# Kernel tuning notes

Hardware: AMD Instinct MI355X
Metric: run time of the kernel (lower is better)

The kernel has to match this reference:

```python
import jax, jax.numpy as jnp
import numpy as np

N_HEADS = 16
HEAD_DIM = 128
ROPE_DIM = 64
ROPE_BASE = 10000.0


def _rope(x, base):
    # x: (B, H, S, dim) -- standard rotate-half RoPE, positions = arange(S)
    B, H, S, dim = x.shape
    inv_freq = 1.0 / (base ** (jnp.arange(0, dim, 2, dtype=jnp.float32) / dim))
    pos = jnp.arange(S, dtype=jnp.float32)
    freqs = pos[:, None] * inv_freq[None, :]                  # (S, dim/2)
    emb = jnp.concatenate([freqs, freqs], axis=-1)            # (S, dim)
    cos = jnp.cos(emb).astype(x.dtype)[None, None]
    sin = jnp.sin(emb).astype(x.dtype)[None, None]
    x1, x2 = x[..., : dim // 2], x[..., dim // 2 :]
    rot = jnp.concatenate([-x2, x1], axis=-1)
    return x * cos + rot * sin


def setup_inputs() -> dict:
    key = jax.random.key(0)
    ks = jax.random.split(key, 7)
    B, S, D = 2, 2048, 2048
    s = 0.02
    return {
        "x": jax.random.normal(ks[0], (B, S, D), jnp.float32),
        "Wq": jax.random.normal(ks[1], (D, N_HEADS * HEAD_DIM), jnp.float32) * s,
        "Wq_rope": jax.random.normal(ks[2], (D, N_HEADS * ROPE_DIM), jnp.float32) * s,
        "Wkv_down": jax.random.normal(ks[3], (D, 512), jnp.float32) * s,
        "Wkv_up": jax.random.normal(ks[4], (512, 2 * N_HEADS * HEAD_DIM), jnp.float32) * s,
        "Wk_rope": jax.random.normal(ks[5], (D, ROPE_DIM), jnp.float32) * s,
        "Wo": jax.random.normal(ks[6], (D, D), jnp.float32) * s,
    }


def reference(x, Wq, Wq_rope, Wkv_down, Wkv_up, Wk_rope, Wo):
    B, S, D = x.shape
    H, hd, rd = N_HEADS, HEAD_DIM, ROPE_DIM

    # content and decoupled-RoPE queries
    q_c = (x @ Wq).reshape(B, S, H, hd).transpose(0, 2, 1, 3)        # (B,H,S,hd)
    q_r = (x @ Wq_rope).reshape(B, S, H, rd).transpose(0, 2, 1, 3)   # (B,H,S,rd)
    q_r = _rope(q_r, ROPE_BASE)

    # low-rank KV latent + shared rope key
    c_kv = x @ Wkv_down                                              # (B,S,r)
    k_r = _rope((x @ Wk_rope)[:, None, :, :], ROPE_BASE)             # (B,1,S,rd)

    kv = c_kv @ Wkv_up                                               # (B,S,2*H*hd)
    k_c, v = jnp.split(kv, 2, axis=-1)
    k_c = k_c.reshape(B, S, H, hd).transpose(0, 2, 1, 3)             # (B,H,S,hd)
    v = v.reshape(B, S, H, hd).transpose(0, 2, 1, 3)                 # (B,H,S,hd)

    q_full = jnp.concatenate([q_c, q_r], axis=-1)                    # (B,H,S,hd+rd)
    k_full = jnp.concatenate([k_c, jnp.broadcast_to(k_r, (B, H, S, rd))], axis=-1)

    scale = 1.0 / np.sqrt(hd + rd).astype(np.float32)
    scores = jnp.einsum("bhqd,bhkd->bhqk", q_full, k_full) * scale   # (B,H,S,S)
    mask = jnp.tril(jnp.ones((S, S), dtype=bool))
    scores = jnp.where(mask[None, None], scores, jnp.finfo(scores.dtype).min)
    attn = jax.nn.softmax(scores, axis=-1)

    out = jnp.einsum("bhqk,bhkd->bhqd", attn, v)                     # (B,H,S,hd)
    out = out.transpose(0, 2, 1, 3).reshape(B, S, D)
    return out @ Wo
```

## Files before the change

### kernel.cpp

```cpp
#include <hip/hip_runtime.h>
#include <hip/hip_bf16.h>
#include <cstdint>
#include <cstddef>

typedef unsigned short u16;
typedef __attribute__((ext_vector_type(8))) short short8;
typedef __attribute__((ext_vector_type(4))) float f32x4;
typedef __attribute__((ext_vector_type(16))) float f32x16;

__device__ __forceinline__ u16 f2bf(float f) {
    union { float f; uint32_t u; } v; v.f = f;
    uint32_t u = v.u;
    return (u16)((u + 0x7fffu + ((u >> 16) & 1u)) >> 16);
}
__device__ __forceinline__ float bf2f(u16 u) {
    union { uint32_t u; float f; } v; v.u = ((uint32_t)u) << 16;
    return v.f;
}
__device__ __forceinline__ float exp2_hw(float x) {
    float r;
    asm("v_exp_f32 %0, %1" : "=v"(r) : "v"(x));
    return r;
}
__device__ __forceinline__ uint32_t cvtpk(float lo, float hi) {
    uint32_t r;
    asm("v_cvt_pk_bf16_f32 %0, %1, %2" : "=v"(r) : "v"(lo), "v"(hi));
    return r;
}
__device__ __forceinline__ void permswap(uint32_t& a, uint32_t& b) {
    asm("v_permlane32_swap_b32 %0, %1" : "+v"(a), "+v"(b));
}
__device__ __forceinline__ float xhalf_max(float x) {
    union { float f; uint32_t u; } a, b; a.f = x; b.f = x;
    permswap(a.u, b.u);
    return fmaxf(a.f, b.f);
}
__device__ __forceinline__ float xhalf_sum(float x) {
    union { float f; uint32_t u; } a, b; a.f = x; b.f = x;
    permswap(a.u, b.u);
    return a.f + b.f;
}

__device__ __forceinline__ void async_cp16(const u16* g, u16* l) {
    __builtin_amdgcn_global_load_lds(
        (const __attribute__((address_space(1))) unsigned int*)g,
        (__attribute__((address_space(3))) unsigned int*)l, 16, 0, 0);
}

__global__ __launch_bounds__(256) void cast_f32_bf16(const float* __restrict__ in,
                                                     u16* __restrict__ out, int n) {
    int i = (blockIdx.x * 256 + threadIdx.x) * 4;
    if (i >= n) return;
    float4 v = *(const float4*)(in + i);
    ushort4 r;
    r.x = f2bf(v.x); r.y = f2bf(v.y); r.z = f2bf(v.z); r.w = f2bf(v.w);
    *(ushort4*)(out + i) = r;
}

__global__ __launch_bounds__(256) void transpose_cast(const float* __restrict__ W,
                                                      u16* __restrict__ Wt, int K, int N,
                                                      float smul) {
    __shared__ u16 tile[64][72];
    int kt = blockIdx.x * 64, nt = blockIdx.y * 64;
    int t = threadIdx.x;
#pragma unroll
    for (int i = 0; i < 16; i++) {
        int idx = t + i * 256; int kl = idx >> 6, nl = idx & 63;
        tile[kl][nl] = f2bf(W[(size_t)(kt + kl) * N + nt + nl] * smul);
    }
    __syncthreads();
#pragma unroll
    for (int i = 0; i < 16; i++) {
        int idx = t + i * 256; int nl = idx >> 6, kl = idx & 63;
        Wt[(size_t)(nt + nl) * K + kt + kl] = tile[kl][nl];
    }
}

template <int OUTF32, int KDIM, int NDIM>
__global__ __launch_bounds__(256) void gemm_bt(const u16* __restrict__ A, int lda,
                                               const u16* __restrict__ Bt,
                                               void* __restrict__ Cout, int ldc) {
    __shared__ __align__(16) u16 Al[128 * 32];
    __shared__ __align__(16) u16 Bl[128 * 32];
    int m0 = blockIdx.x * 128, n0 = blockIdx.y * 128;
    int t = threadIdx.x;
    int w = t >> 6, l = t & 63;
    int lm = l & 15, lq = l >> 4;
    int wm = (w >> 1) * 64, wn = (w & 1) * 64;
    f32x4 acc[4][4] = {};

    for (int k0 = 0; k0 < KDIM; k0 += 32) {
#pragma unroll
        for (int c = 0; c < 2; c++) {
            int chunk = w * 128 + c * 64 + l;
            int row = chunk >> 2, col8 = (chunk & 3) * 8;
            async_cp16(A + (size_t)(m0 + row) * lda + k0 + col8,
                       Al + (w * 128 + c * 64) * 8);
            int brow = n0 + row;
            if (NDIM % 128 != 0) { if (brow >= NDIM) brow = NDIM - 1; }
            async_cp16(Bt + (size_t)brow * KDIM + k0 + col8,
                       Bl + (w * 128 + c * 64) * 8);
        }
        __syncthreads();
        short8 af[4], bfr[4];
#pragma unroll
        for (int mt = 0; mt < 4; mt++)
            af[mt] = *(const short8*)(Al + (wm + mt * 16 + lm) * 32 + lq * 8);
#pragma unroll
        for (int nt = 0; nt < 4; nt++)
            bfr[nt] = *(const short8*)(Bl + (wn + nt * 16 + lm) * 32 + lq * 8);
#pragma unroll
        for (int mt = 0; mt < 4; mt++)
#pragma unroll
            for (int nt = 0; nt < 4; nt++)
                acc[mt][nt] = __builtin_amdgcn_mfma_f32_16x16x32_bf16(af[mt], bfr[nt], acc[mt][nt], 0, 0, 0);
        __syncthreads();
    }
#pragma unroll
    for (int mt = 0; mt < 4; mt++) {
#pragma unroll
        for (int nt = 0; nt < 4; nt++) {
            int col = n0 + wn + nt * 16 + lm;
            if (col < NDIM) {
#pragma unroll
                for (int r = 0; r < 4; r++) {
                    int row = m0 + wm + mt * 16 + lq * 4 + r;
                    if (OUTF32) ((float*)Cout)[(size_t)row * ldc + col] = acc[mt][nt][r];
                    else        ((u16*)Cout)[(size_t)row * ldc + col] = f2bf(acc[mt][nt][r]);
                }
            }
        }
    }
}

__global__ __launch_bounds__(256) void rope_kernel(u16* __restrict__ x, int rows,
                                                   int nheads, int Smask, int stride) {
    int i = blockIdx.x * 256 + threadIdx.x;
    int total = rows * nheads * 32;
    if (i >= total) return;
    int j = i & 31;
    int h = (i >> 5) % nheads;
    int row = i / (32 * nheads);
    int pos = row & Smask;
    float f = exp2f((float)j * -0.4152410118609828f);
    float ang = (float)pos * f;
    float c = cosf(ang), s = sinf(ang);
    u16* p = x + (size_t)row * stride + h * 64 + j;
    float x1 = bf2f(p[0]), x2 = bf2f(p[32]);
    p[0]  = f2bf(x1 * c - x2 * s);
    p[32] = f2bf(x2 * c + x1 * s);
}

__global__ __launch_bounds__(256) void transpose_v(const u16* __restrict__ kv,
                                                   u16* __restrict__ vt, int S) {
    __shared__ u16 tile[64][72];
    int bh = blockIdx.z; int b = bh >> 4, h = bh & 15;
    int s0 = blockIdx.x * 64, d0 = blockIdx.y * 64;
    int t = threadIdx.x;
#pragma unroll
    for (int i = 0; i < 16; i++) {
        int idx = t + i * 256; int sl = idx >> 6, dl = idx & 63;
        tile[sl][dl] = kv[(size_t)(b * S + s0 + sl) * 4096 + 2048 + h * 128 + d0 + dl];
    }
    __syncthreads();
#pragma unroll
    for (int i = 0; i < 16; i++) {
        int idx = t + i * 256; int dl = idx >> 6, sl = idx & 63;
        vt[((size_t)(bh * 128 + d0 + dl)) * S + s0 + sl] = tile[sl][dl];
    }
}

__global__ __launch_bounds__(256, 2) void mla_attn(const u16* __restrict__ qc, int qcs,
                                                   const u16* __restrict__ qr, int qrs,
                                                   const u16* __restrict__ kvbuf,
                                                   const u16* __restrict__ kr, int krs,
                                                   const u16* __restrict__ vt,
                                                   u16* __restrict__ out, int S) {
    __shared__ __align__(16) u16 Kl[64 * 200];
    __shared__ __align__(16) u16 Vl[128 * 72];
    const float NEG = -1e30f;
    int bh = blockIdx.x; int b = bh >> 4, h = bh & 15;
    int y = blockIdx.y;
    int qt = (y < 8) ? (15 - y) : (y - 8);
    int t = threadIdx.x, w = t >> 6, l = t & 63;
    int ln = l & 31, hi = l >> 5;

    short8 kreg[6], vreg[4];
    auto load_tile = [&](int kbase) {
#pragma unroll
        for (int c = 0; c < 6; c++) {
            int idx = t + c * 256;
            int row = idx / 24, col = (idx % 24) * 8;
            const u16* src = (col < 128)
                ? kvbuf + (size_t)(b * S + kbase + row) * 4096 + h * 128 + col
                : kr + (size_t)(b * S + kbase + row) * krs + (col - 128);
            kreg[c] = *(const short8*)src;
        }
#pragma unroll
        for (int c = 0; c < 4; c++) {
            int idx = t + c * 256;
            int row = idx >> 3, col = (idx & 7) * 8;
            vreg[c] = *(const short8*)(vt + ((size_t)bh * 128 + row) * S + kbase + col);
        }
    };

    int qrow = qt * 128 + w * 32;
    int ntiles = 2 * qt + 2;

    short8 bq[12];
    {
        const u16* qc_row = qc + (size_t)(b * S + qrow + ln) * qcs + h * 128;
#pragma unroll
        for (int ks = 0; ks < 8; ks++) bq[ks] = *(const short8*)(qc_row + ks * 16 + hi * 8);
        const u16* qr_row = qr + (size_t)(b * S + qrow + ln) * qrs + h * 64;
#pragma unroll
        for (int ks = 0; ks < 4; ks++) bq[8 + ks] = *(const short8*)(qr_row + ks * 16 + hi * 8);
    }

    f32x16 o[4] = {};
    float m_s = 0.0f, l_s = 0.f;

    load_tile(0);
    for (int kt = 0; kt < ntiles; kt++) {
        int kbase = kt * 64;
        __syncthreads();
#pragma unroll
        for (int c = 0; c < 6; c++) {
            int idx = t + c * 256;
            int row = idx / 24, col = (idx % 24) * 8;
            *(short8*)(Kl + row * 200 + col) = kreg[c];
        }
#pragma unroll
        for (int c = 0; c < 4; c++) {
            int idx = t + c * 256;
            int row = idx >> 3, col = (idx & 7) * 8;
            *(short8*)(Vl + row * 72 + col) = vreg[c];
        }
        __syncthreads();
        if (kt + 1 < ntiles) load_tile(kbase + 64);

        if (kbase > qrow + 31) continue;

        f32x16 sacc[2] = {};
        __builtin_amdgcn_s_setprio(1);
#pragma unroll
        for (int ks = 0; ks < 12; ks++) {
            short8 ak0 = *(const short8*)(Kl + ln * 200 + ks * 16 + hi * 8);
            short8 ak1 = *(const short8*)(Kl + (32 + ln) * 200 + ks * 16 + hi * 8);
            sacc[0] = __builtin_amdgcn_mfma_f32_32x32x16_bf16(ak0, bq[ks], sacc[0], 0, 0, 0);
            sacc[1] = __builtin_amdgcn_mfma_f32_32x32x16_bf16(ak1, bq[ks], sacc[1], 0, 0, 0);
        }
        __builtin_amdgcn_s_setprio(0);

        if (kbase + 63 > qrow) {
            int qi = qrow + ln;
#pragma unroll
            for (int kt2 = 0; kt2 < 2; kt2++)
#pragma unroll
                for (int r = 0; r < 16; r++) {
                    int key = kbase + kt2 * 32 + (r & 3) + 8 * (r >> 2) + 4 * hi;
                    if (key > qi) sacc[kt2][r] = NEG;
                }
        }

        float m01 = NEG, m23 = NEG;
#pragma unroll
        for (int r = 0; r < 16; r += 2) {
            m01 = fmaxf(m01, fmaxf(sacc[0][r], sacc[0][r + 1]));
            m23 = fmaxf(m23, fmaxf(sacc[1][r], sacc[1][r + 1]));
        }
        float mx = xhalf_max(fmaxf(m01, m23));
        if (!__all(mx - m_s <= 8.0f)) {
            float mnew = fmaxf(m_s, mx);
            float alpha = exp2_hw(m_s - mnew);
            m_s = mnew;
            l_s *= alpha;
#pragma unroll
            for (int dt = 0; dt < 4; dt++) o[dt] *= alpha;
        }

        float rs = 0.f;
        short8 bp[2][2];
#pragma unroll
        for (int kt2 = 0; kt2 < 2; kt2++) {
            float p[16];
#pragma unroll
            for (int r = 0; r < 16; r++) p[r] = exp2_hw(sacc[kt2][r] - m_s);
#pragma unroll
            for (int r = 0; r < 16; r += 4)
                rs += (p[r] + p[r + 1]) + (p[r + 2] + p[r + 3]);
            uint32_t c0 = cvtpk(p[0], p[1]),  c1 = cvtpk(p[2], p[3]);
            uint32_t c2 = cvtpk(p[4], p[5]),  c3 = cvtpk(p[6], p[7]);
            permswap(c0, c2); permswap(c1, c3);
            union { uint32_t u[4]; short8 s; } f0 = {{c0, c1, c2, c3}};
            bp[kt2][0] = f0.s;
            uint32_t c4 = cvtpk(p[8], p[9]),   c5 = cvtpk(p[10], p[11]);
            uint32_t c6 = cvtpk(p[12], p[13]), c7 = cvtpk(p[14], p[15]);
            permswap(c4, c6); permswap(c5, c7);
            union { uint32_t u[4]; short8 s; } f1 = {{c4, c5, c6, c7}};
            bp[kt2][1] = f1.s;
        }
        l_s += xhalf_sum(rs);

        __builtin_amdgcn_s_setprio(1);
#pragma unroll
        for (int kt2 = 0; kt2 < 2; kt2++)
#pragma unroll
            for (int s = 0; s < 2; s++)
#pragma unroll
                for (int dt = 0; dt < 4; dt++) {
                    short8 av = *(const short8*)(Vl + (dt * 32 + ln) * 72 + kt2 * 32 + s * 16 + hi * 8);
                    o[dt] = __builtin_amdgcn_mfma_f32_32x32x16_bf16(av, bp[kt2][s], o[dt], 0, 0, 0);
                }
        __builtin_amdgcn_s_setprio(0);
    }

    float inv = 1.0f / l_s;
    u16* orow = out + (size_t)(b * S + qrow + ln) * 2048 + h * 128;
#pragma unroll
    for (int dt = 0; dt < 4; dt++)
#pragma unroll
        for (int g = 0; g < 4; g++) {
            ushort4 pk4;
            pk4.x = f2bf(o[dt][g * 4 + 0] * inv);
            pk4.y = f2bf(o[dt][g * 4 + 1] * inv);
            pk4.z = f2bf(o[dt][g * 4 + 2] * inv);
            pk4.w = f2bf(o[dt][g * 4 + 3] * inv);
            *(ushort4*)(orow + dt * 32 + g * 8 + hi * 4) = pk4;
        }
}

extern "C" void kernel_launch(void* const* d_in, const int* in_sizes, int n_in,
                              void* d_out, int out_size, void* d_ws, size_t ws_size,
                              hipStream_t stream) {
    const int B = 2, S = 2048, D = 2048, H = 16;
    const int M = B * S;
    const int NP = 3648;
    const int NPpad = 3712;
    const float scale = 0.07216878364870323f * 1.4426950408889634f;
    const float* x    = (const float*)d_in[0];
    const float* Wq   = (const float*)d_in[1];
    const float* Wqr  = (const float*)d_in[2];
    const float* Wkvd = (const float*)d_in[3];
    const float* Wkvu = (const float*)d_in[4];
    const float* Wkr  = (const float*)d_in[5];
    const float* Wo   = (const float*)d_in[6];

    u16* p = (u16*)d_ws;
    u16* xb     = p; p += (size_t)M * D;
    u16* WprojT = p; p += (size_t)NPpad * 2048;
    u16* WkvuT  = p; p += (size_t)4096 * 512;
    u16* WoT    = p; p += (size_t)2048 * 2048;
    u16* proj   = p; p += (size_t)M * NPpad;
    u16* kv     = p; p += (size_t)M * 4096;
    u16* v_t    = p; p += (size_t)B * H * 128 * S;
    u16* attn   = p; p += (size_t)M * 2048;

    u16* q_c = proj;
    u16* q_r = proj + 2048;
    u16* ckv = proj + 3072;
    u16* k_r = proj + 3584;

    cast_f32_bf16<<<(M * D) / 4 / 256, 256, 0, stream>>>(x, xb, M * D);
    transpose_cast<<<dim3(32, 32), 256, 0, stream>>>(Wq,   WprojT,               2048, 2048, scale);
    transpose_cast<<<dim3(32, 16), 256, 0, stream>>>(Wqr,  WprojT + 2048 * 2048, 2048, 1024, scale);
    transpose_cast<<<dim3(32, 8),  256, 0, stream>>>(Wkvd, WprojT + 3072 * 2048, 2048, 512, 1.0f);
    transpose_cast<<<dim3(32, 1),  256, 0, stream>>>(Wkr,  WprojT + 3584 * 2048, 2048, 64, 1.0f);
    transpose_cast<<<dim3(8, 64),  256, 0, stream>>>(Wkvu, WkvuT, 512, 4096, 1.0f);
    transpose_cast<<<dim3(32, 32), 256, 0, stream>>>(Wo,   WoT,   2048, 2048, 1.0f);

    gemm_bt<0, 2048, NP><<<dim3(32, 29), 256, 0, stream>>>(xb, 2048, WprojT, proj, NPpad);

    rope_kernel<<<(M * 16 * 32) / 256, 256, 0, stream>>>(q_r, M, 16, S - 1, NPpad);
    rope_kernel<<<(M * 32) / 256, 256, 0, stream>>>(k_r, M, 1, S - 1, NPpad);

    gemm_bt<0, 512, 4096><<<dim3(32, 32), 256, 0, stream>>>(ckv, NPpad, WkvuT, kv, 4096);
    transpose_v<<<dim3(32, 2, 32), 256, 0, stream>>>(kv, v_t, S);

    mla_attn<<<dim3(32, 16), 256, 0, stream>>>(q_c, NPpad, q_r, NPpad, kv, k_r, NPpad,
                                               v_t, attn, S);

    gemm_bt<1, 2048, 2048><<<dim3(32, 16), 256, 0, stream>>>(attn, 2048, WoT, d_out, 2048);
}
```

Before: 397.4 us.

## Add 256x256-tile pipelined GEMM for projection and KV-up GEMMs

```diff
diff --git a/kernel.cpp b/kernel.cpp
--- a/kernel.cpp
+++ b/kernel.cpp
@@ -131,6 +131,78 @@
             }
         }
     }
+}
+
+template <int KDIM>
+__global__ __launch_bounds__(512, 2) void gemm256(const u16* __restrict__ A, int lda,
+                                                  const u16* __restrict__ Bt,
+                                                  u16* __restrict__ C, int ldc) {
+    __shared__ __align__(16) u16 Ab[4][256 * 32];
+    __shared__ __align__(16) u16 Bb[4][256 * 32];
+    const int nk = KDIM / 32;
+    int m0 = blockIdx.x * 256, n0 = blockIdx.y * 256;
+    int t = threadIdx.x, w = t >> 6, l = t & 63;
+    int lm = l & 15, lq = l >> 4;
+    int wm = (w >> 2) * 128, wn = (w & 3) * 64;
+
+    int c1 = t + 512;
+    int ar0 = t >> 2,  as0 = (((t >> 0) & 3) ^ ((ar0 >> 1) & 3)) * 8;
+    int ar1 = c1 >> 2, as1 = ((c1 & 3) ^ ((ar1 >> 1) & 3)) * 8;
+    const u16* Ap0 = A + (size_t)(m0 + ar0) * lda + as0;
+    const u16* Ap1 = A + (size_t)(m0 + ar1) * lda + as1;
+    const u16* Bp0 = Bt + (size_t)(n0 + ar0) * KDIM + as0;
+    const u16* Bp1 = Bt + (size_t)(n0 + ar1) * KDIM + as1;
+    int dst0 = (w * 64) * 8;
+    int dst1 = (w * 64 + 512) * 8;
+
+    auto stage = [&](int ks) {
+        int buf = ks & 3, ko = ks * 32;
+        async_cp16(Ap0 + ko, Ab[buf] + dst0);
+        async_cp16(Ap1 + ko, Ab[buf] + dst1);
+        async_cp16(Bp0 + ko, Bb[buf] + dst0);
+        async_cp16(Bp1 + ko, Bb[buf] + dst1);
+    };
+
+    int slot = (lq ^ ((lm >> 1) & 3)) * 8;
+
+    f32x4 acc[8][4] = {};
+    stage(0); stage(1);
+    asm volatile("s_waitcnt vmcnt(4)" ::: "memory");
+    __builtin_amdgcn_s_barrier();
+
+    for (int ks = 0; ks < nk; ks++) {
+        if (ks + 2 < nk) stage(ks + 2);
+        const u16* Al = Ab[ks & 3];
+        const u16* Bl = Bb[ks & 3];
+        short8 bfr[4], af[8];
+#pragma unroll
+        for (int nt = 0; nt < 4; nt++)
+            bfr[nt] = *(const short8*)(Bl + (wn + nt * 16 + lm) * 32 + slot);
+#pragma unroll
+        for (int mt = 0; mt < 8; mt++)
+            af[mt] = *(const short8*)(Al + (wm + mt * 16 + lm) * 32 + slot);
+        __builtin_amdgcn_s_setprio(1);
+#pragma unroll
+        for (int mt = 0; mt < 8; mt++)
+#pragma unroll
+            for (int nt = 0; nt < 4; nt++)
+                acc[mt][nt] = __builtin_amdgcn_mfma_f32_16x16x32_bf16(af[mt], bfr[nt], acc[mt][nt], 0, 0, 0);
+        __builtin_amdgcn_s_setprio(0);
+        if (ks + 2 < nk)      { asm volatile("s_waitcnt vmcnt(4)" ::: "memory"); }
+        else if (ks + 1 < nk) { asm volatile("s_waitcnt vmcnt(0)" ::: "memory"); }
+        if (ks + 1 < nk) __builtin_amdgcn_s_barrier();
+    }
+
+#pragma unroll
+    for (int mt = 0; mt < 8; mt++)
+#pragma unroll
+        for (int nt = 0; nt < 4; nt++) {
+            int col = n0 + wn + nt * 16 + lm;
+            u16* cp = C + (size_t)(m0 + wm + mt * 16 + lq * 4) * ldc + col;
+#pragma unroll
+            for (int r = 0; r < 4; r++)
+                cp[(size_t)r * ldc] = f2bf(acc[mt][nt][r]);
+        }
 }
 
 __global__ __launch_bounds__(256) void rope_kernel(u16* __restrict__ x, int rows,
@@ -335,8 +407,7 @@
                               hipStream_t stream) {
     const int B = 2, S = 2048, D = 2048, H = 16;
     const int M = B * S;
-    const int NP = 3648;
-    const int NPpad = 3712;
+    const int NPpad = 3840;
     const float scale = 0.07216878364870323f * 1.4426950408889634f;
     const float* x    = (const float*)d_in[0];
     const float* Wq   = (const float*)d_in[1];
@@ -369,12 +440,12 @@
     transpose_cast<<<dim3(8, 64),  256, 0, stream>>>(Wkvu, WkvuT, 512, 4096, 1.0f);
     transpose_cast<<<dim3(32, 32), 256, 0, stream>>>(Wo,   WoT,   2048, 2048, 1.0f);
 
-    gemm_bt<0, 2048, NP><<<dim3(32, 29), 256, 0, stream>>>(xb, 2048, WprojT, proj, NPpad);
+    gemm256<2048><<<dim3(16, 15), 512, 0, stream>>>(xb, 2048, WprojT, proj, NPpad);
 
     rope_kernel<<<(M * 16 * 32) / 256, 256, 0, stream>>>(q_r, M, 16, S - 1, NPpad);
     rope_kernel<<<(M * 32) / 256, 256, 0, stream>>>(k_r, M, 1, S - 1, NPpad);
 
-    gemm_bt<0, 512, 4096><<<dim3(32, 32), 256, 0, stream>>>(ckv, NPpad, WkvuT, kv, 4096);
+    gemm256<512><<<dim3(16, 16), 512, 0, stream>>>(ckv, NPpad, WkvuT, kv, 4096);
     transpose_v<<<dim3(32, 2, 32), 256, 0, stream>>>(kv, v_t, S);
 
     mla_attn<<<dim3(32, 16), 256, 0, stream>>>(q_c, NPpad, q_r, NPpad, kv, k_r, NPpad,
```

New measurement: 384.4 us. 3.3% less time.
